# Performance work log

Measured on AMD Instinct MI355X. Metric: run time of the kernel, lower is better.

## Reference

```python
import jax, jax.numpy as jnp
import numpy as np

K = 3          # kernel_size
STRIDE = 1
PAD = 1
BASIS = 8      # act_fun.get_size() (Hermite basis order)


def _unfold(x):
    # x: [B, Cin, H, W] -> patches [B, Cin, K*K, L] (same ordering as F.unfold)
    b, c, h, w = x.shape
    p = jax.lax.conv_general_dilated_patches(
        x, filter_shape=(K, K), window_strides=(STRIDE, STRIDE),
        padding=[(PAD, PAD), (PAD, PAD)])
    # p: [B, Cin*K*K, Hout, Wout], channel-major ordering (Cin, Kh, Kw)
    ho, wo = p.shape[2], p.shape[3]
    return p.reshape(b, c, K * K, ho * wo), ho, wo


def _hermite(x):
    # Physicists' Hermite polynomials H_0..H_{BASIS-1}, stacked on last axis.
    hs = [jnp.ones_like(x), 2.0 * x]
    for n in range(1, BASIS - 1):
        hs.append(2.0 * x * hs[n] - 2.0 * n * hs[n - 1])
    return jnp.stack(hs[:BASIS], axis=-1)


def setup_inputs() -> dict:
    key = jax.random.key(0)
    k1, k2, k3, k4 = jax.random.split(key, 4)
    cin, cout = 64, 128
    x = jax.random.normal(k1, (16, cin, 32, 32), dtype=jnp.float32)
    # xavier_normal on [Cin,Cout,K^2,1]: std = sqrt(2/(fan_in+fan_out)) over last two dims -> use small randn
    w_b = jax.random.normal(k2, (cin, cout, K * K, 1), dtype=jnp.float32)
    w_s = jax.random.normal(k3, (cin, cout, K * K, 1), dtype=jnp.float32) * 0.001
    c = jax.random.normal(k4, (cin, cout, K * K, 1, BASIS), dtype=jnp.float32) * 0.1
    return {"x": x, "w_b": w_b, "w_s": w_s, "c": c}


def reference(x, w_b, w_s, c):
    b = x.shape[0]
    xw, ho, wo = _unfold(x)                      # [B, Cin, K2, L]
    phi = _hermite(xw)                           # [B, Cin, K2, L, BASIS]
    res = jax.nn.silu(xw)                        # residual activation
    # effective spline weight: w_s * c, contracted over Cin, K2, basis
    cw = w_s[..., 0, None] * c[:, :, :, 0, :]    # [Cin, Cout, K2, BASIS]
    out = (jnp.einsum('ioka,bikla->bol', cw, phi)
           + jnp.einsum('iok,bikl->bol', w_b[..., 0], res))  # [B, Cout, L]
    return out.reshape(b, -1, ho, wo)
```

## Files before the change

### kernel.cpp

```cpp
#include <hip/hip_runtime.h>
#include <stdint.h>

typedef unsigned short ushort_t;
typedef short short8 __attribute__((ext_vector_type(8)));
typedef float f32x4 __attribute__((ext_vector_type(4)));

#define CIN   64
#define COUT  128
#define BATCH 16
#define LPIX  1024
#define NTOT  (BATCH*LPIX)
#define C2N   576
#define PIXN  (BATCH*34*34)
#define NSTEP2 72
#define KS    4
#define PART_ELEMS (NTOT*COUT)
#define FEAT_BLOCKS (PIXN/4)
#define WPREP_BLOCKS 128

#define FEAT_BYTES (PIXN*C2N*2)
#define W_OFF      FEAT_BYTES
#define W_BYTES    (COUT*NSTEP2*64*2)
#define BIAS_OFF   (W_OFF + W_BYTES)
#define PART_OFF   (BIAS_OFF + 512)
#define PART_BYTES (PART_ELEMS*2)
#define WS_NEED    ((size_t)PART_OFF + (size_t)KS*PART_BYTES)

#define VM0() asm volatile("s_waitcnt vmcnt(0)" ::: "memory")
#define BAR() __builtin_amdgcn_s_barrier()

__device__ __forceinline__ ushort_t to_bf16(float f) {
  union { float f; uint32_t u; } v; v.f = f;
  uint32_t r = (v.u + 0x7fffu + ((v.u >> 16) & 1u)) >> 16;
  return (ushort_t)r;
}
__device__ __forceinline__ float from_bf16(ushort_t u) {
  union { uint32_t u; float f; } v; v.u = ((uint32_t)u) << 16;
  return v.f;
}

__device__ __forceinline__ void basis9(float x, float* o) {
  float hm = 1.f, h = 2.f * x;
  o[0] = hm; o[1] = h;
#pragma unroll
  for (int n = 1; n < 7; ++n) {
    float nx = 2.f * x * h - 2.f * (float)n * hm;
    hm = h; h = nx;
    o[n + 1] = nx;
  }
  o[8] = x / (1.f + __expf(-x));
}

__device__ __forceinline__ void load16(const void* g, void* l) {
  __builtin_amdgcn_global_load_lds(
      (const __attribute__((address_space(1))) uint32_t*)g,
      (__attribute__((address_space(3))) uint32_t*)l, 16, 0, 0);
}

__global__ void prep_kernel(const float* __restrict__ x, ushort_t* __restrict__ feat,
                            const float* __restrict__ wb, const float* __restrict__ wsp,
                            const float* __restrict__ cc, ushort_t* __restrict__ W,
                            float* __restrict__ bias) {
  const int t = threadIdx.x;
  if (blockIdx.x < WPREP_BLOCKS) {
    __shared__ ushort_t wl[NSTEP2 * 64];
    const int m = blockIdx.x;
    if (t < 64) {
      const int i = t;
      const int base = (i * COUT + m) * 9;
      const int r = ((((i >> 3) & 7) ^ (m & 7)) << 3) | (i & 7);
      float h0 = 0.f;
#pragma unroll
      for (int kk = 0; kk < 9; ++kk) {
        const float ws_ = wsp[base + kk];
        const float wbv = wb[base + kk];
        const float* cp = cc + (size_t)(base + kk) * 8;
        h0 += ws_ * cp[0];
#pragma unroll
        for (int sf = 1; sf <= 8; ++sf) {
          const float val = (sf < 8) ? ws_ * cp[sf] : wbv;
          wl[((sf - 1) * 9 + kk) * 64 + r] = to_bf16(val);
        }
      }
#pragma unroll
      for (int off = 32; off > 0; off >>= 1) h0 += __shfl_down(h0, off, 64);
      if (t == 0) bias[m] = h0;
    }
    __syncthreads();
    uint32_t* dst = (uint32_t*)&W[(size_t)m * (NSTEP2 * 64)];
    const uint32_t* src = (const uint32_t*)wl;
#pragma unroll
    for (int jj = 0; jj < 9; ++jj) dst[jj * 256 + t] = src[jj * 256 + t];
  } else {
    const int lane = t & 63;
    const int pg = (blockIdx.x - WPREP_BLOCKS) * 4 + (t >> 6);
    const int xx = pg % 34;
    const int rest = pg / 34;
    const int yy = rest % 34;
    const int bb = rest / 34;
    float v = 0.f;
    if (xx >= 1 && xx <= 32 && yy >= 1 && yy <= 32)
      v = x[((bb * CIN + lane) * 32 + (yy - 1)) * 32 + (xx - 1)];
    float o[9];
    basis9(v, o);
    ushort_t* dst = feat + (size_t)pg * C2N + lane;
#pragma unroll
    for (int f = 1; f < 9; ++f) dst[f * 64] = to_bf16(o[f]);
  }
}

__global__ __launch_bounds__(256, 2) void gemm_kernel(const ushort_t* __restrict__ feat,
                                                      const ushort_t* __restrict__ W,
                                                      ushort_t* __restrict__ part) {
  __shared__ f32x4 smem4[76288 / 16];
  ushort_t (*Ab)[4096] = (ushort_t(*)[4096])smem4;
  ushort_t* Hb = (ushort_t*)smem4 + 16384;
  const int t = threadIdx.x;
  const int lane = t & 63;
  const int wn = t >> 6;

  const int logical = (blockIdx.x & 7) * 64 + (blockIdx.x >> 3);
  const int nb = logical >> 3;
  const int rem = logical & 7;
  const int mt = rem >> 2;
  const int ksplit = rem & 3;
  const int lo = ksplit * 18;

  const int b  = nb >> 2;
  const int y0 = (nb & 3) * 8;
  const int pixbase = (b * 34 + y0) * 34;

  const char* Wb = (const char*)W + mt * 64 * (NSTEP2 * 64 * 2);
  const char* Fb = (const char*)feat;

  f32x4 acc[4][4];
#pragma unroll
  for (int a = 0; a < 4; ++a)
#pragma unroll
    for (int c = 0; c < 4; ++c) acc[a][c] = (f32x4)0.f;

  auto stage_halo = [&](int c2s) {
    const char* base = Fb + (size_t)pixbase * (C2N * 2) + (c2s + 1) * 128;
#pragma unroll
    for (int it = 0; it < 11; ++it) {
      const int q = it * 256 + t;
      if (q < 2720) {
        const int L = q >> 3;
        const int sl = (q & 7) ^ (L & 7);
        load16(base + L * (C2N * 2) + (sl << 4), &Hb[q * 8]);
      }
    }
  };

  auto stageA = [&](int p, int s) {
#pragma unroll
    for (int q = 0; q < 2; ++q) {
      const int idx16 = q * 256 + t;
      const int m = idx16 >> 3, ccn = idx16 & 7;
      load16(Wb + m * (NSTEP2 * 64 * 2) + s * 128 + ccn * 16, &Ab[p][idx16 * 8]);
    }
  };

  auto compute = [&](int p, int j) {
    const int dy = j / 3, dx = j - dy * 3;
#pragma unroll
    for (int ks = 0; ks < 2; ++ks) {
      short8 av[4], bv[4];
      const int kslot = ks * 4 + (lane >> 4);
#pragma unroll
      for (int mf = 0; mf < 4; ++mf) {
        const int row = mf * 16 + (lane & 15);
        av[mf] = *(const short8*)&Ab[p][row * 64 + ((kslot ^ (row & 7)) << 3)];
      }
#pragma unroll
      for (int nf = 0; nf < 4; ++nf) {
        const int nl = wn * 64 + nf * 16 + (lane & 15);
        const int L = ((nl >> 5) + dy) * 34 + (nl & 31) + dx;
        bv[nf] = *(const short8*)&Hb[L * 64 + ((kslot ^ (L & 7)) << 3)];
      }
      __builtin_amdgcn_s_setprio(1);
#pragma unroll
      for (int mf = 0; mf < 4; ++mf)
#pragma unroll
        for (int nf = 0; nf < 4; ++nf)
          acc[mf][nf] = __builtin_amdgcn_mfma_f32_16x16x32_bf16(av[mf], bv[nf],
                                                                acc[mf][nf], 0, 0, 0);
      __builtin_amdgcn_s_setprio(0);
    }
  };

  stage_halo(2 * ksplit);
  stageA(0, lo + 0);
  stageA(1, lo + 1);

  VM0(); BAR(); stageA(2, lo + 2);  stageA(3, lo + 3);  compute(0, 0); compute(1, 1);
  VM0(); BAR(); stageA(0, lo + 4);  stageA(1, lo + 5);  compute(2, 2); compute(3, 3);
  VM0(); BAR(); stageA(2, lo + 6);  stageA(3, lo + 7);  compute(0, 4); compute(1, 5);
  VM0(); BAR(); stageA(0, lo + 8);  stageA(1, lo + 9);  compute(2, 6); compute(3, 7);
  VM0(); BAR();                                         compute(0, 8);
  BAR(); stage_halo(2 * ksplit + 1); stageA(2, lo + 10);
  VM0(); BAR(); stageA(3, lo + 11); stageA(0, lo + 12); compute(1, 0); compute(2, 1);
  VM0(); BAR(); stageA(1, lo + 13); stageA(2, lo + 14); compute(3, 2); compute(0, 3);
  VM0(); BAR(); stageA(3, lo + 15); stageA(0, lo + 16); compute(1, 4); compute(2, 5);
  VM0(); BAR(); stageA(1, lo + 17);                     compute(3, 6); compute(0, 7);
  VM0(); BAR();                                         compute(1, 8);

  BAR();
  float* scr = (float*)smem4 + wn * 4352;
#pragma unroll
  for (int mf = 0; mf < 4; ++mf)
#pragma unroll
    for (int nf = 0; nf < 4; ++nf)
#pragma unroll
      for (int rg = 0; rg < 4; ++rg)
        scr[(mf * 16 + (lane >> 4) * 4 + rg) * 68 + nf * 16 + (lane & 15)] =
            acc[mf][nf][rg];
  ushort_t* dst = part + (size_t)ksplit * PART_ELEMS;
#pragma unroll
  for (int it = 0; it < 8; ++it) {
    const int row = it * 8 + (lane >> 3);
    const int c0 = (lane & 7) * 8;
    const float* p = &scr[row * 68 + c0];
    short8 v;
#pragma unroll
    for (int e = 0; e < 8; ++e) v[e] = (short)to_bf16(p[e]);
    const int m = mt * 64 + row;
    const int n = nb * 256 + wn * 64 + c0;
    const int bb = n >> 10, ll = n & 1023;
    __builtin_nontemporal_store(v, (short8*)&dst[(bb * COUT + m) * LPIX + ll]);
  }
}

__global__ void add_kernel(float* __restrict__ out, const ushort_t* __restrict__ part,
                           const float* __restrict__ bias) {
  const int i = (blockIdx.x * 256 + threadIdx.x) * 8;
  const float bv = bias[(i >> 10) & 127];
  f32x4 a0 = (f32x4)bv;
  f32x4 a1 = (f32x4)bv;
#pragma unroll
  for (int j = 0; j < KS; ++j) {
    const short8 pv = __builtin_nontemporal_load(
        (const short8*)&part[(size_t)j * PART_ELEMS + i]);
#pragma unroll
    for (int e = 0; e < 4; ++e) {
      a0[e] += from_bf16((ushort_t)pv[e]);
      a1[e] += from_bf16((ushort_t)pv[e + 4]);
    }
  }
  __builtin_nontemporal_store(a0, (f32x4*)&out[i]);
  __builtin_nontemporal_store(a1, (f32x4*)&out[i + 4]);
}

__global__ void naive_kernel(const float* __restrict__ x, const float* __restrict__ wb,
                             const float* __restrict__ wsp, const float* __restrict__ cc,
                             float* __restrict__ out) {
  const int idx = blockIdx.x * 256 + threadIdx.x;
  if (idx >= BATCH * COUT * LPIX) return;
  const int l = idx & 1023, o = (idx >> 10) & 127, b = idx >> 17;
  const int h = l >> 5, w = l & 31;
  float acc = 0.f;
  for (int i = 0; i < CIN; ++i)
    for (int kk = 0; kk < 9; ++kk) {
      const int yy = h + kk / 3 - 1, xx = w + kk % 3 - 1;
      const float v = (yy >= 0 && yy < 32 && xx >= 0 && xx < 32)
                          ? x[((b * CIN + i) * 32 + yy) * 32 + xx] : 0.f;
      float ftr[9];
      basis9(v, ftr);
      const int base = (i * COUT + o) * 9 + kk;
      const float* cp = cc + base * 8;
      float dot = 0.f;
#pragma unroll
      for (int f = 0; f < 8; ++f) dot += cp[f] * ftr[f];
      acc += wsp[base] * dot + wb[base] * ftr[8];
    }
  out[idx] = acc;
}

extern "C" void kernel_launch(void* const* d_in, const int* in_sizes, int n_in,
                              void* d_out, int out_size, void* d_ws, size_t ws_size,
                              hipStream_t stream) {
  const float* x  = (const float*)d_in[0];
  const float* wb = (const float*)d_in[1];
  const float* wsp = (const float*)d_in[2];
  const float* cc = (const float*)d_in[3];
  float* out = (float*)d_out;

  if (ws_size < WS_NEED) {
    naive_kernel<<<(BATCH * COUT * LPIX + 255) / 256, 256, 0, stream>>>(x, wb, wsp, cc, out);
    return;
  }

  char* ws = (char*)d_ws;
  ushort_t* feat = (ushort_t*)ws;
  ushort_t* W    = (ushort_t*)(ws + W_OFF);
  float* bias    = (float*)(ws + BIAS_OFF);
  ushort_t* part = (ushort_t*)(ws + PART_OFF);

  prep_kernel<<<WPREP_BLOCKS + FEAT_BLOCKS, 256, 0, stream>>>(x, feat, wb, wsp, cc, W, bias);
  gemm_kernel<<<64 * 2 * KS, 256, 0, stream>>>(feat, W, part);
  add_kernel<<<PART_ELEMS / 2048, 256, 0, stream>>>(out, part, bias);
}
```

Baseline: 38.76 us.

## Coalesce feature-prep input reads via LDS transpose with 64 pixels per block

The feature-prep branch now handles 64 pixels per block instead of 4. Each thread reads 16 channels of x for its pixel, so consecutive threads load consecutive pixels and the reads coalesce. The Hermite and SiLU basis values go through a padded LDS tile and are written back channel-contiguous. This removes the strided per-channel loads of the old mapping, at the cost of 16 barriers per block and more registers per thread.

```diff
diff --git a/kernel.cpp b/kernel.cpp
--- a/kernel.cpp
+++ b/kernel.cpp
@@ -15,7 +15,7 @@
 #define NSTEP2 72
 #define KS    4
 #define PART_ELEMS (NTOT*COUT)
-#define FEAT_BLOCKS (PIXN/4)
+#define FEAT_BLOCKS (PIXN/64)
 #define WPREP_BLOCKS 128
 
 #define FEAT_BYTES (PIXN*C2N*2)
@@ -92,20 +92,46 @@
 #pragma unroll
     for (int jj = 0; jj < 9; ++jj) dst[jj * 256 + t] = src[jj * 256 + t];
   } else {
+    __shared__ ushort_t fl[64][66];
+    const int pg0 = (blockIdx.x - WPREP_BLOCKS) * 64;
+    const int px = t & 63;
+    const int cg = t >> 6;
     const int lane = t & 63;
-    const int pg = (blockIdx.x - WPREP_BLOCKS) * 4 + (t >> 6);
+    const int pg = pg0 + px;
     const int xx = pg % 34;
     const int rest = pg / 34;
     const int yy = rest % 34;
     const int bb = rest / 34;
-    float v = 0.f;
-    if (xx >= 1 && xx <= 32 && yy >= 1 && yy <= 32)
-      v = x[((bb * CIN + lane) * 32 + (yy - 1)) * 32 + (xx - 1)];
-    float o[9];
-    basis9(v, o);
-    ushort_t* dst = feat + (size_t)pg * C2N + lane;
-#pragma unroll
-    for (int f = 1; f < 9; ++f) dst[f * 64] = to_bf16(o[f]);
+    const bool inb = (xx >= 1 && xx <= 32 && yy >= 1 && yy <= 32);
+    const float* xbase = x + (((bb * CIN) * 32 + (yy - 1)) * 32 + (xx - 1));
+    float vv[16], h[16], hm[16];
+#pragma unroll
+    for (int ccn = 0; ccn < 16; ++ccn) {
+      const int ch = cg * 16 + ccn;
+      vv[ccn] = inb ? xbase[ch * LPIX] : 0.f;
+      hm[ccn] = 1.f;
+      h[ccn] = 2.f * vv[ccn];
+    }
+#pragma unroll
+    for (int f = 1; f <= 8; ++f) {
+#pragma unroll
+      for (int ccn = 0; ccn < 16; ++ccn) {
+        const float o = (f == 8) ? (vv[ccn] / (1.f + __expf(-vv[ccn]))) : h[ccn];
+        fl[px][cg * 16 + ccn] = to_bf16(o);
+        if (f < 8) {
+          const float nx = 2.f * vv[ccn] * h[ccn] - 2.f * (float)f * hm[ccn];
+          hm[ccn] = h[ccn];
+          h[ccn] = nx;
+        }
+      }
+      __syncthreads();
+#pragma unroll
+      for (int r = 0; r < 16; ++r) {
+        const int row = cg * 16 + r;
+        feat[(size_t)(pg0 + row) * C2N + f * 64 + lane] = fl[row][lane];
+      }
+      __syncthreads();
+    }
   }
 }
 
```

After: 39.91 us. 1.03x slower.
